# Kernel tuning notes

Measured on AMD Instinct MI355X. Metric: run time of the kernel, lower is better.

The kernel has to match this reference:

```python
import jax, jax.numpy as jnp
import numpy as np

N_NODES = 50000
N_EDGES = 800000
DIM = 128
N_LAYERS = 3
N_GRAPHS = 64
NEG_SLOPE = 0.2


def setup_inputs() -> dict:
    key = jax.random.key(0)
    ks = jax.random.split(key, 9)
    x = jax.random.normal(ks[0], (N_NODES, DIM), dtype=jnp.float32)
    edge_index = jax.random.randint(ks[1], (2, N_EDGES), 0, N_NODES, dtype=jnp.int32)
    batch = jnp.sort(jax.random.randint(ks[2], (N_NODES,), 0, N_GRAPHS, dtype=jnp.int32))
    Ws = jax.random.normal(ks[3], (N_LAYERS, DIM, DIM), dtype=jnp.float32) / np.sqrt(DIM)
    att_src = jax.random.normal(ks[4], (N_LAYERS, DIM), dtype=jnp.float32) * 0.1
    att_dst = jax.random.normal(ks[5], (N_LAYERS, DIM), dtype=jnp.float32) * 0.1
    biases = jnp.zeros((N_LAYERS, DIM), dtype=jnp.float32)
    Wf = jax.random.normal(ks[6], (DIM, 1), dtype=jnp.float32) / np.sqrt(DIM)
    bf = jnp.zeros((1,), dtype=jnp.float32)
    return {"x": x, "edge_index": edge_index, "batch": batch, "Ws": Ws,
            "att_src": att_src, "att_dst": att_dst, "biases": biases,
            "Wf": Wf, "bf": bf}


def _gat_layer(x, src, dst, W, a_src, a_dst, b, n_nodes):
    # PyG GATConv, heads=1: linear transform, per-edge attention, softmax over
    # edges incoming to each dst node, scatter-add aggregation, bias.
    h = x @ W                                        # [N, H]
    alpha = jax.nn.leaky_relu(
        (h * a_src).sum(-1)[src] + (h * a_dst).sum(-1)[dst], NEG_SLOPE)  # [E]
    m = jax.ops.segment_max(alpha, dst, num_segments=n_nodes)
    e = jnp.exp(alpha - m[dst])
    s = jax.ops.segment_sum(e, dst, num_segments=n_nodes)
    w = e / (s[dst] + 1e-16)                         # softmax per dst-neighborhood
    out = jax.ops.segment_sum(w[:, None] * h[src], dst, num_segments=n_nodes)
    return out + b


def reference(x, edge_index, batch, Ws, att_src, att_dst, biases, Wf, bf):
    n_nodes = x.shape[0]
    loop = jnp.arange(n_nodes, dtype=edge_index.dtype)   # add_self_loops=True
    src = jnp.concatenate([edge_index[0], loop])
    dst = jnp.concatenate([edge_index[1], loop])
    for l in range(N_LAYERS):
        x = _gat_layer(x, src, dst, Ws[l], att_src[l], att_dst[l], biases[l], n_nodes)
        x = jax.nn.relu(x)
    pooled = jax.ops.segment_sum(x, batch, num_segments=N_GRAPHS)  # global_add_pool
    y = (pooled @ Wf + bf).squeeze(-1)               # [N_GRAPHS]
    return y
```

## Files before the change

kernel.cpp:

```cpp
#include <hip/hip_runtime.h>
#include <hip/hip_bf16.h>

#define N_NODES 50000
#define DIM 128
#define N_GRAPHS 64
#define E_RAW 800000
#define E_TOT 850000
#define NSLOT 1000000
#define E_CAP 1200000
#define NEG_SLOPE 0.2f
#define PAD_SENT 0xFFFF0000u

typedef unsigned int uint;
typedef unsigned short ushort;
typedef float v2f __attribute__((ext_vector_type(2)));
typedef short bf16x8 __attribute__((ext_vector_type(8)));
typedef float f32x4 __attribute__((ext_vector_type(4)));

__device__ __forceinline__ int pi_pos(int p) {
    return (p >> 3) + 32 * ((p >> 1) & 3) + 16 * (p & 1);
}

__device__ __forceinline__ ushort f2bf(float f) {
    uint u = __float_as_uint(f);
    u += 0x7fffu + ((u >> 16) & 1u);
    return (ushort)(u >> 16);
}

__global__ void init_kernel(int* deg, int* fillc, float* pooled) {
    int i = blockIdx.x * blockDim.x + threadIdx.x;
    if (i < N_NODES) { deg[i] = 0; fillc[i] = 0; }
    if (i < N_GRAPHS * DIM) pooled[i] = 0.f;
}

__global__ void csr_init_kernel(uint* __restrict__ csr) {
    int i = blockIdx.x * blockDim.x + threadIdx.x;
    if (i < NSLOT / 4) ((uint4*)csr)[i] = make_uint4(PAD_SENT, PAD_SENT, PAD_SENT, PAD_SENT);
}

__global__ void x2bf_kernel(const float* __restrict__ x, ushort* __restrict__ xb) {
    int i = blockIdx.x * blockDim.x + threadIdx.x;
    if (i >= N_NODES * DIM / 4) return;
    float4 v = ((const float4*)x)[i];
    ushort4 o;
    o.x = f2bf(v.x); o.y = f2bf(v.y); o.z = f2bf(v.z); o.w = f2bf(v.w);
    ((ushort4*)xb)[i] = o;
}

__global__ void wprep_kernel(const float* __restrict__ Ws, ushort* __restrict__ Wfrag) {
    int t = blockIdx.x * blockDim.x + threadIdx.x;
    if (t >= 3 * 32 * 64) return;
    int l = t >> 11;
    int rem = t & 2047;
    int chunk = rem >> 6, lane = rem & 63;
    int ks = chunk >> 3, nt = chunk & 7;
    int cc = lane & 15, gg = lane >> 4;
    const float* W = Ws + (size_t)l * DIM * DIM;
    ushort o[8];
#pragma unroll
    for (int j = 0; j < 8; ++j) {
        int kp = ks * 32 + gg * 8 + j;
        int kl = (l == 0) ? kp : pi_pos(kp);
        o[j] = f2bf(W[kl * DIM + nt * 16 + cc]);
    }
#pragma unroll
    for (int j = 0; j < 8; ++j) Wfrag[(size_t)t * 8 + j] = o[j];
}

__global__ void count_kernel(const int* __restrict__ ei, int* __restrict__ deg) {
    int e = blockIdx.x * blockDim.x + threadIdx.x;
    if (e >= E_TOT) return;
    int dst = (e < E_RAW) ? ei[E_RAW + e] : (e - E_RAW);
    atomicAdd(&deg[dst], 1);
}

__global__ void scan1_kernel(const int* __restrict__ deg, int* __restrict__ excl,
                             int* __restrict__ blksum, int n) {
    __shared__ int lds[256];
    int t = threadIdx.x;
    int i = blockIdx.x * 256 + t;
    int v = (i < n) ? ((deg[i] + 3) & ~3) : 0;
    lds[t] = v;
    __syncthreads();
    int incl = v;
    for (int off = 1; off < 256; off <<= 1) {
        int y = (t >= off) ? lds[t - off] : 0;
        __syncthreads();
        incl += y;
        lds[t] = incl;
        __syncthreads();
    }
    if (i < n) excl[i] = incl - v;
    if (t == 255) blksum[blockIdx.x] = incl;
}

__global__ void scan2_kernel(int* __restrict__ blksum, int* __restrict__ row_ptr, int nblk) {
    __shared__ int lds[256];
    int t = threadIdx.x;
    int v = (t < nblk) ? blksum[t] : 0;
    lds[t] = v;
    __syncthreads();
    int incl = v;
    for (int off = 1; off < 256; off <<= 1) {
        int y = (t >= off) ? lds[t - off] : 0;
        __syncthreads();
        incl += y;
        lds[t] = incl;
        __syncthreads();
    }
    if (t < nblk) blksum[t] = incl - v;
    if (t == nblk - 1) row_ptr[N_NODES] = incl;
}

__global__ void scan3_kernel(int* __restrict__ row_ptr, const int* __restrict__ blksum, int n) {
    int i = blockIdx.x * blockDim.x + threadIdx.x;
    if (i < n) row_ptr[i] += blksum[i >> 8];
}

__global__ void fill_kernel(const int* __restrict__ ei, const int* __restrict__ row_ptr,
                            int* __restrict__ fillc, uint* __restrict__ csr) {
    int e = blockIdx.x * blockDim.x + threadIdx.x;
    if (e >= E_TOT) return;
    int src, dst;
    if (e < E_RAW) { src = ei[e]; dst = ei[E_RAW + e]; }
    else           { src = dst = e - E_RAW; }
    int slot = row_ptr[dst] + atomicAdd(&fillc[dst], 1);
    csr[slot] = (uint)src | ((uint)dst << 16);
}

__global__ __launch_bounds__(256) void gemm_mfma_kernel(
    const ushort* __restrict__ Xb, const ushort* __restrict__ Wfrag,
    const float* __restrict__ asrc, const float* __restrict__ adst,
    uint* __restrict__ Hb, float* __restrict__ s1, float* __restrict__ s2, int nrows) {
    int wv = threadIdx.x >> 6;
    int lane = threadIdx.x & 63;
    int c = lane & 15, g = lane >> 4;
    int row0 = blockIdx.x * 64 + wv * 16;

    int arow = row0 + c;
    if (arow >= nrows) arow = nrows - 1;
    const ushort* xrow = Xb + (size_t)arow * DIM;

    f32x4 acc[8];
#pragma unroll
    for (int nt = 0; nt < 8; ++nt) acc[nt] = (f32x4)(0.f);

#pragma unroll
    for (int ks = 0; ks < 4; ++ks) {
        bf16x8 afrag = *(const bf16x8*)(xrow + ks * 32 + g * 8);
#pragma unroll
        for (int nt = 0; nt < 8; ++nt) {
            bf16x8 bfrag = *(const bf16x8*)(Wfrag + ((size_t)(ks * 8 + nt) * 64 + lane) * 8);
            acc[nt] = __builtin_amdgcn_mfma_f32_16x16x32_bf16(afrag, bfrag, acc[nt], 0, 0, 0);
        }
    }

    float a1[8], a2[8];
#pragma unroll
    for (int nt = 0; nt < 8; ++nt) { a1[nt] = asrc[c + 16 * nt]; a2[nt] = adst[c + 16 * nt]; }

#pragma unroll
    for (int r = 0; r < 4; ++r) {
        int outrow = row0 + g * 4 + r;
        bool valid = outrow < nrows;
        if (valid) {
            int w0 = __builtin_amdgcn_cvt_pk_fp8_f32(acc[0][r], acc[1][r], 0, false);
            w0     = __builtin_amdgcn_cvt_pk_fp8_f32(acc[2][r], acc[3][r], w0, true);
            int w1 = __builtin_amdgcn_cvt_pk_fp8_f32(acc[4][r], acc[5][r], 0, false);
            w1     = __builtin_amdgcn_cvt_pk_fp8_f32(acc[6][r], acc[7][r], w1, true);
            *(uint2*)&Hb[(size_t)outrow * 32 + c * 2] = make_uint2((uint)w0, (uint)w1);
        }
        float p1 = 0.f, p2 = 0.f;
#pragma unroll
        for (int nt = 0; nt < 8; ++nt) {
            p1 = fmaf(acc[nt][r], a1[nt], p1);
            p2 = fmaf(acc[nt][r], a2[nt], p2);
        }
#pragma unroll
        for (int m = 1; m < 16; m <<= 1) { p1 += __shfl_xor(p1, m); p2 += __shfl_xor(p2, m); }
        if (c == 0 && valid) { s1[outrow] = p1; s2[outrow] = p2; }
    }
}

__global__ __launch_bounds__(256) void ew_kernel(
    const uint* __restrict__ csr, const float* __restrict__ s1,
    const float* __restrict__ s2, float* __restrict__ w) {
    int i = blockIdx.x * blockDim.x + threadIdx.x;
    if (i >= NSLOT / 4) return;
    uint4 e = ((const uint4*)csr)[i];
    uint ev[4] = {e.x, e.y, e.z, e.w};
    float ov[4];
#pragma unroll
    for (int j = 0; j < 4; ++j) {
        uint dv = ev[j] >> 16;
        uint sv = ev[j] & 0xFFFFu;
        float wv = 0.f;
        if (dv != 0xFFFFu) {
            float al = s1[sv] + s2[dv];
            al = fmaxf(al, NEG_SLOPE * al);
            wv = __expf(al);
        }
        ov[j] = wv;
    }
    float4 o;
    o.x = ov[0]; o.y = ov[1]; o.z = ov[2]; o.w = ov[3];
    ((float4*)w)[i] = o;
}

__global__ __launch_bounds__(256) void agg_kernel(
    const uint2* __restrict__ Hb2, const uint* __restrict__ csr,
    const int* __restrict__ row_ptr, const float* __restrict__ w,
    const float* __restrict__ bias,
    ushort* __restrict__ Xout, const int* __restrict__ batch,
    float* __restrict__ pooled, int pool_flag, int ngroups) {
    int gw = (blockIdx.x * blockDim.x + threadIdx.x) >> 6;
    int lane = threadIdx.x & 63;
    if (gw >= ngroups) return;
    int node0 = gw * 8;
    int ql = lane & 15;
    int grp = lane >> 4;

    int4 rpa = *(const int4*)&row_ptr[node0];
    int4 rpb = *(const int4*)&row_ptr[node0 + 4];
    int rp8 = row_ptr[node0 + 8];
    int rp[9] = {rpa.x, rpa.y, rpa.z, rpa.w, rpb.x, rpb.y, rpb.z, rpb.w, rp8};

    int p0 = 8 * ql + 2 * grp;
    float2 b2;
    b2.x = bias[pi_pos(p0)];
    b2.y = bias[pi_pos(p0) + 16];

    int ba[8] = {0, 0, 0, 0, 0, 0, 0, 0};
    if (pool_flag) {
        int4 bqa = *(const int4*)&batch[node0];
        int4 bqb = *(const int4*)&batch[node0 + 4];
        ba[0] = bqa.x; ba[1] = bqa.y; ba[2] = bqa.z; ba[3] = bqa.w;
        ba[4] = bqb.x; ba[5] = bqb.y; ba[6] = bqb.z; ba[7] = bqb.w;
    }

#pragma unroll
    for (int k = 0; k < 8; ++k) {
        int beg = rp[k], end = rp[k + 1];
        float a0 = 0.f, a1 = 0.f, a2 = 0.f, a3 = 0.f;
        float a4 = 0.f, a5 = 0.f, a6 = 0.f, a7 = 0.f, ws = 0.f;

        for (int s = beg; s < end; s += 8) {
            uint4 ca = *(const uint4*)&csr[s];
            float4 wa = *(const float4*)&w[s];
            bool vb = (s + 4) < end;
            uint4 cb = vb ? *(const uint4*)&csr[s + 4]
                          : make_uint4(PAD_SENT, PAD_SENT, PAD_SENT, PAD_SENT);
            float4 wb = vb ? *(const float4*)&w[s + 4] : make_float4(0.f, 0.f, 0.f, 0.f);

            uint  eA = (grp == 0) ? ca.x : (grp == 1) ? ca.y : (grp == 2) ? ca.z : ca.w;
            float wA = (grp == 0) ? wa.x : (grp == 1) ? wa.y : (grp == 2) ? wa.z : wa.w;
            uint  eB = (grp == 0) ? cb.x : (grp == 1) ? cb.y : (grp == 2) ? cb.z : cb.w;
            float wB = (grp == 0) ? wb.x : (grp == 1) ? wb.y : (grp == 2) ? wb.z : wb.w;

            uint2 hA = Hb2[(eA & 0xFFFFu) * 16u + (uint)ql];
            uint2 hB = Hb2[(eB & 0xFFFFu) * 16u + (uint)ql];

            v2f f;
            f = __builtin_amdgcn_cvt_pk_f32_fp8((int)hA.x, false); a0 = fmaf(wA, f.x, a0); a1 = fmaf(wA, f.y, a1);
            f = __builtin_amdgcn_cvt_pk_f32_fp8((int)hA.x, true);  a2 = fmaf(wA, f.x, a2); a3 = fmaf(wA, f.y, a3);
            f = __builtin_amdgcn_cvt_pk_f32_fp8((int)hA.y, false); a4 = fmaf(wA, f.x, a4); a5 = fmaf(wA, f.y, a5);
            f = __builtin_amdgcn_cvt_pk_f32_fp8((int)hA.y, true);  a6 = fmaf(wA, f.x, a6); a7 = fmaf(wA, f.y, a7);
            ws += wA;
            f = __builtin_amdgcn_cvt_pk_f32_fp8((int)hB.x, false); a0 = fmaf(wB, f.x, a0); a1 = fmaf(wB, f.y, a1);
            f = __builtin_amdgcn_cvt_pk_f32_fp8((int)hB.x, true);  a2 = fmaf(wB, f.x, a2); a3 = fmaf(wB, f.y, a3);
            f = __builtin_amdgcn_cvt_pk_f32_fp8((int)hB.y, false); a4 = fmaf(wB, f.x, a4); a5 = fmaf(wB, f.y, a5);
            f = __builtin_amdgcn_cvt_pk_f32_fp8((int)hB.y, true);  a6 = fmaf(wB, f.x, a6); a7 = fmaf(wB, f.y, a7);
            ws += wB;
        }

        a0 += __shfl_xor(a0, 16); a0 += __shfl_xor(a0, 32);
        a1 += __shfl_xor(a1, 16); a1 += __shfl_xor(a1, 32);
        a2 += __shfl_xor(a2, 16); a2 += __shfl_xor(a2, 32);
        a3 += __shfl_xor(a3, 16); a3 += __shfl_xor(a3, 32);
        a4 += __shfl_xor(a4, 16); a4 += __shfl_xor(a4, 32);
        a5 += __shfl_xor(a5, 16); a5 += __shfl_xor(a5, 32);
        a6 += __shfl_xor(a6, 16); a6 += __shfl_xor(a6, 32);
        a7 += __shfl_xor(a7, 16); a7 += __shfl_xor(a7, 32);
        ws += __shfl_xor(ws, 16); ws += __shfl_xor(ws, 32);

        float inv = 1.f / (ws + 1e-16f);
        float vx = (grp == 0) ? a0 : (grp == 1) ? a2 : (grp == 2) ? a4 : a6;
        float vy = (grp == 0) ? a1 : (grp == 1) ? a3 : (grp == 2) ? a5 : a7;
        vx = fmaxf(fmaf(vx, inv, b2.x), 0.f);
        vy = fmaxf(fmaf(vy, inv, b2.y), 0.f);

        if (pool_flag) {
            atomicAdd(&pooled[ba[k] * DIM + p0], vx);
            atomicAdd(&pooled[ba[k] * DIM + p0 + 1], vy);
        } else {
            ushort2 hb;
            hb.x = f2bf(vx);
            hb.y = f2bf(vy);
            ((ushort2*)Xout)[(size_t)(node0 + k) * 64 + (p0 >> 1)] = hb;
        }
    }
}

__global__ void final_kernel(const float* __restrict__ pooled, const float* __restrict__ Wf,
                             const float* __restrict__ bf, float* __restrict__ y) {
    int wid = (blockIdx.x * blockDim.x + threadIdx.x) >> 6;
    int lane = threadIdx.x & 63;
    if (wid >= N_GRAPHS) return;
    float2 p = *(const float2*)&pooled[wid * DIM + 2 * lane];
    int cc = lane >> 2, ii = lane & 3;
    float wx = Wf[cc + 32 * ii];
    float wy = Wf[cc + 32 * ii + 16];
    float v = p.x * wx + p.y * wy;
    for (int off = 32; off; off >>= 1) v += __shfl_down(v, off);
    if (lane == 0) y[wid] = v + bf[0];
}

extern "C" void kernel_launch(void* const* d_in, const int* in_sizes, int n_in,
                              void* d_out, int out_size, void* d_ws, size_t ws_size,
                              hipStream_t stream) {
    const float* x       = (const float*)d_in[0];
    const int*   ei      = (const int*)d_in[1];
    const int*   batch   = (const int*)d_in[2];
    const float* Ws      = (const float*)d_in[3];
    const float* att_src = (const float*)d_in[4];
    const float* att_dst = (const float*)d_in[5];
    const float* biases  = (const float*)d_in[6];
    const float* Wf      = (const float*)d_in[7];
    const float* bf      = (const float*)d_in[8];
    float* y = (float*)d_out;

    char* p = (char*)d_ws;
    auto alloc = [&](size_t bytes) -> void* {
        void* r = (void*)p;
        p += (bytes + 255) & ~(size_t)255;
        return r;
    };
    ushort* xC     = (ushort*)alloc((size_t)(N_NODES + 64) * DIM * 2);
    ushort* xA     = (ushort*)alloc((size_t)(N_NODES + 64) * DIM * 2);
    uint*   Hb     = (uint*)alloc((size_t)N_NODES * 32 * 4);
    ushort* Wfrag  = (ushort*)alloc((size_t)3 * 32 * 64 * 8 * 2);
    uint*  csr     = (uint*)alloc((size_t)E_CAP * 4);
    float* wbuf    = (float*)alloc((size_t)E_CAP * 4);
    int*   deg     = (int*)alloc((size_t)N_NODES * 4);
    int*   fillc   = (int*)alloc((size_t)N_NODES * 4);
    int*   row_ptr = (int*)alloc((size_t)(N_NODES + 16) * 4);
    int*   blksum  = (int*)alloc(256 * 4);
    float* s1      = (float*)alloc((size_t)N_NODES * 4);
    float* s2      = (float*)alloc((size_t)(N_NODES + 8) * 4);
    float* pooled  = (float*)alloc((size_t)N_GRAPHS * DIM * 4);

    const int BN = 256;
    const int gN   = (N_NODES + BN - 1) / BN;
    const int gE   = (E_TOT + BN - 1) / BN;
    const int ngroups = N_NODES / 8;
    const int gAGG = (ngroups * 64 + BN - 1) / BN;
    const int nblk = gN;
    const int gCVT = (N_NODES * DIM / 4 + BN - 1) / BN;
    const int gGEMM = (N_NODES + 63) / 64;
    const int gEW  = (NSLOT / 4 + BN - 1) / BN;
    const int gCI  = (NSLOT / 4 + BN - 1) / BN;

    init_kernel<<<gN, BN, 0, stream>>>(deg, fillc, pooled);
    csr_init_kernel<<<gCI, BN, 0, stream>>>(csr);
    x2bf_kernel<<<gCVT, BN, 0, stream>>>(x, xC);
    wprep_kernel<<<(3 * 32 * 64 + BN - 1) / BN, BN, 0, stream>>>(Ws, Wfrag);
    count_kernel<<<gE, BN, 0, stream>>>(ei, deg);
    scan1_kernel<<<nblk, BN, 0, stream>>>(deg, row_ptr, blksum, N_NODES);
    scan2_kernel<<<1, BN, 0, stream>>>(blksum, row_ptr, nblk);
    scan3_kernel<<<gN, BN, 0, stream>>>(row_ptr, blksum, N_NODES);
    fill_kernel<<<gE, BN, 0, stream>>>(ei, row_ptr, fillc, csr);

    const ushort* xin = xC;
    ushort* xout = xA;
    for (int l = 0; l < 3; ++l) {
        const ushort* Wf_l = Wfrag + (size_t)l * 32 * 64 * 8;
        const float* as = att_src + (size_t)l * DIM;
        const float* ad = att_dst + (size_t)l * DIM;
        const float* b  = biases + (size_t)l * DIM;

        gemm_mfma_kernel<<<gGEMM, BN, 0, stream>>>(xin, Wf_l, as, ad, Hb, s1, s2, N_NODES);
        ew_kernel<<<gEW, BN, 0, stream>>>(csr, s1, s2, wbuf);
        agg_kernel<<<gAGG, BN, 0, stream>>>((const uint2*)Hb, csr, row_ptr, wbuf, b,
                                            xout, batch, pooled,
                                            (l == 2) ? 1 : 0, ngroups);
        xin = xout;
        xout = (l == 0) ? xC : xA;
    }

    final_kernel<<<(N_GRAPHS * 64 + BN - 1) / BN, BN, 0, stream>>>(pooled, Wf, bf, y);
    (void)ws_size; (void)n_in; (void)in_sizes; (void)out_size;
}
```

Before: 354.5 us.

## Pack bf16 edge weight with source index and restructure aggregation loop

The edge-weight kernel now writes a single packed word per edge (source index in the low 16 bits, bf16 weight in the high 16), so the aggregation kernel reads one stream instead of separate csr and weight arrays. The aggregation loop now handles 4 edges per iteration, prefetching the next packed chunk, instead of 8 with a conditional second load. Each wave now covers 4 nodes rather than 8, which doubles the wave count. This cuts edge-stream traffic and the selects for the second chunk, but weights lose precision going to bf16 and there are fewer independent gathers in flight per iteration.

```diff
diff --git a/kernel.cpp b/kernel.cpp
--- a/kernel.cpp
+++ b/kernel.cpp
@@ -184,93 +184,75 @@
 
 __global__ __launch_bounds__(256) void ew_kernel(
     const uint* __restrict__ csr, const float* __restrict__ s1,
-    const float* __restrict__ s2, float* __restrict__ w) {
+    const float* __restrict__ s2, uint* __restrict__ cw) {
     int i = blockIdx.x * blockDim.x + threadIdx.x;
     if (i >= NSLOT / 4) return;
     uint4 e = ((const uint4*)csr)[i];
     uint ev[4] = {e.x, e.y, e.z, e.w};
-    float ov[4];
+    uint ov[4];
 #pragma unroll
     for (int j = 0; j < 4; ++j) {
         uint dv = ev[j] >> 16;
         uint sv = ev[j] & 0xFFFFu;
-        float wv = 0.f;
+        uint out = 0u;
         if (dv != 0xFFFFu) {
             float al = s1[sv] + s2[dv];
             al = fmaxf(al, NEG_SLOPE * al);
-            wv = __expf(al);
-        }
-        ov[j] = wv;
-    }
-    float4 o;
-    o.x = ov[0]; o.y = ov[1]; o.z = ov[2]; o.w = ov[3];
-    ((float4*)w)[i] = o;
+            float wv = __expf(al);
+            out = sv | ((uint)f2bf(wv) << 16);
+        }
+        ov[j] = out;
+    }
+    ((uint4*)cw)[i] = make_uint4(ov[0], ov[1], ov[2], ov[3]);
 }
 
 __global__ __launch_bounds__(256) void agg_kernel(
-    const uint2* __restrict__ Hb2, const uint* __restrict__ csr,
-    const int* __restrict__ row_ptr, const float* __restrict__ w,
-    const float* __restrict__ bias,
+    const uint2* __restrict__ Hb2, const uint* __restrict__ cw,
+    const int* __restrict__ row_ptr, const float* __restrict__ bias,
     ushort* __restrict__ Xout, const int* __restrict__ batch,
     float* __restrict__ pooled, int pool_flag, int ngroups) {
     int gw = (blockIdx.x * blockDim.x + threadIdx.x) >> 6;
     int lane = threadIdx.x & 63;
     if (gw >= ngroups) return;
-    int node0 = gw * 8;
+    int node0 = gw * 4;
     int ql = lane & 15;
     int grp = lane >> 4;
 
     int4 rpa = *(const int4*)&row_ptr[node0];
-    int4 rpb = *(const int4*)&row_ptr[node0 + 4];
-    int rp8 = row_ptr[node0 + 8];
-    int rp[9] = {rpa.x, rpa.y, rpa.z, rpa.w, rpb.x, rpb.y, rpb.z, rpb.w, rp8};
+    int rp4 = row_ptr[node0 + 4];
 
     int p0 = 8 * ql + 2 * grp;
     float2 b2;
     b2.x = bias[pi_pos(p0)];
     b2.y = bias[pi_pos(p0) + 16];
 
-    int ba[8] = {0, 0, 0, 0, 0, 0, 0, 0};
+    int ba0 = 0, ba1 = 0, ba2 = 0, ba3 = 0;
     if (pool_flag) {
-        int4 bqa = *(const int4*)&batch[node0];
-        int4 bqb = *(const int4*)&batch[node0 + 4];
-        ba[0] = bqa.x; ba[1] = bqa.y; ba[2] = bqa.z; ba[3] = bqa.w;
-        ba[4] = bqb.x; ba[5] = bqb.y; ba[6] = bqb.z; ba[7] = bqb.w;
-    }
-
-#pragma unroll
-    for (int k = 0; k < 8; ++k) {
-        int beg = rp[k], end = rp[k + 1];
+        int4 bq = *(const int4*)&batch[node0];
+        ba0 = bq.x; ba1 = bq.y; ba2 = bq.z; ba3 = bq.w;
+    }
+
+    auto seg = [&](int beg, int end, int bk, int node) {
         float a0 = 0.f, a1 = 0.f, a2 = 0.f, a3 = 0.f;
         float a4 = 0.f, a5 = 0.f, a6 = 0.f, a7 = 0.f, ws = 0.f;
 
-        for (int s = beg; s < end; s += 8) {
-            uint4 ca = *(const uint4*)&csr[s];
-            float4 wa = *(const float4*)&w[s];
-            bool vb = (s + 4) < end;
-            uint4 cb = vb ? *(const uint4*)&csr[s + 4]
-                          : make_uint4(PAD_SENT, PAD_SENT, PAD_SENT, PAD_SENT);
-            float4 wb = vb ? *(const float4*)&w[s + 4] : make_float4(0.f, 0.f, 0.f, 0.f);
-
-            uint  eA = (grp == 0) ? ca.x : (grp == 1) ? ca.y : (grp == 2) ? ca.z : ca.w;
-            float wA = (grp == 0) ? wa.x : (grp == 1) ? wa.y : (grp == 2) ? wa.z : wa.w;
-            uint  eB = (grp == 0) ? cb.x : (grp == 1) ? cb.y : (grp == 2) ? cb.z : cb.w;
-            float wB = (grp == 0) ? wb.x : (grp == 1) ? wb.y : (grp == 2) ? wb.z : wb.w;
-
-            uint2 hA = Hb2[(eA & 0xFFFFu) * 16u + (uint)ql];
-            uint2 hB = Hb2[(eB & 0xFFFFu) * 16u + (uint)ql];
+        uint4 cur = *(const uint4*)&cw[beg];
+        for (int s = beg; s < end; s += 4) {
+            int snx = s + 4;
+            snx = (snx < end) ? snx : s;
+            uint4 nxt = *(const uint4*)&cw[snx];
+
+            uint  e  = (grp == 0) ? cur.x : (grp == 1) ? cur.y : (grp == 2) ? cur.z : cur.w;
+            float wv = __uint_as_float(e & 0xFFFF0000u);
+            uint2 hv = Hb2[(e & 0xFFFFu) * 16u + (uint)ql];
 
             v2f f;
-            f = __builtin_amdgcn_cvt_pk_f32_fp8((int)hA.x, false); a0 = fmaf(wA, f.x, a0); a1 = fmaf(wA, f.y, a1);
-            f = __builtin_amdgcn_cvt_pk_f32_fp8((int)hA.x, true);  a2 = fmaf(wA, f.x, a2); a3 = fmaf(wA, f.y, a3);
-            f = __builtin_amdgcn_cvt_pk_f32_fp8((int)hA.y, false); a4 = fmaf(wA, f.x, a4); a5 = fmaf(wA, f.y, a5);
-            f = __builtin_amdgcn_cvt_pk_f32_fp8((int)hA.y, true);  a6 = fmaf(wA, f.x, a6); a7 = fmaf(wA, f.y, a7);
-            ws += wA;
-            f = __builtin_amdgcn_cvt_pk_f32_fp8((int)hB.x, false); a0 = fmaf(wB, f.x, a0); a1 = fmaf(wB, f.y, a1);
-            f = __builtin_amdgcn_cvt_pk_f32_fp8((int)hB.x, true);  a2 = fmaf(wB, f.x, a2); a3 = fmaf(wB, f.y, a3);
-            f = __builtin_amdgcn_cvt_pk_f32_fp8((int)hB.y, false); a4 = fmaf(wB, f.x, a4); a5 = fmaf(wB, f.y, a5);
-            f = __builtin_amdgcn_cvt_pk_f32_fp8((int)hB.y, true);  a6 = fmaf(wB, f.x, a6); a7 = fmaf(wB, f.y, a7);
-            ws += wB;
+            f = __builtin_amdgcn_cvt_pk_f32_fp8((int)hv.x, false); a0 = fmaf(wv, f.x, a0); a1 = fmaf(wv, f.y, a1);
+            f = __builtin_amdgcn_cvt_pk_f32_fp8((int)hv.x, true);  a2 = fmaf(wv, f.x, a2); a3 = fmaf(wv, f.y, a3);
+            f = __builtin_amdgcn_cvt_pk_f32_fp8((int)hv.y, false); a4 = fmaf(wv, f.x, a4); a5 = fmaf(wv, f.y, a5);
+            f = __builtin_amdgcn_cvt_pk_f32_fp8((int)hv.y, true);  a6 = fmaf(wv, f.x, a6); a7 = fmaf(wv, f.y, a7);
+            ws += wv;
+            cur = nxt;
         }
 
         a0 += __shfl_xor(a0, 16); a0 += __shfl_xor(a0, 32);
@@ -290,15 +272,20 @@
         vy = fmaxf(fmaf(vy, inv, b2.y), 0.f);
 
         if (pool_flag) {
-            atomicAdd(&pooled[ba[k] * DIM + p0], vx);
-            atomicAdd(&pooled[ba[k] * DIM + p0 + 1], vy);
+            atomicAdd(&pooled[bk * DIM + p0], vx);
+            atomicAdd(&pooled[bk * DIM + p0 + 1], vy);
         } else {
             ushort2 hb;
             hb.x = f2bf(vx);
             hb.y = f2bf(vy);
-            ((ushort2*)Xout)[(size_t)(node0 + k) * 64 + (p0 >> 1)] = hb;
-        }
-    }
+            ((ushort2*)Xout)[(size_t)node * 64 + (p0 >> 1)] = hb;
+        }
+    };
+
+    seg(rpa.x, rpa.y, ba0, node0);
+    seg(rpa.y, rpa.z, ba1, node0 + 1);
+    seg(rpa.z, rpa.w, ba2, node0 + 2);
+    seg(rpa.w, rp4,  ba3, node0 + 3);
 }
 
 __global__ void final_kernel(const float* __restrict__ pooled, const float* __restrict__ Wf,
@@ -340,7 +327,7 @@
     uint*   Hb     = (uint*)alloc((size_t)N_NODES * 32 * 4);
     ushort* Wfrag  = (ushort*)alloc((size_t)3 * 32 * 64 * 8 * 2);
     uint*  csr     = (uint*)alloc((size_t)E_CAP * 4);
-    float* wbuf    = (float*)alloc((size_t)E_CAP * 4);
+    uint*  cwbuf   = (uint*)alloc((size_t)E_CAP * 4);
     int*   deg     = (int*)alloc((size_t)N_NODES * 4);
     int*   fillc   = (int*)alloc((size_t)N_NODES * 4);
     int*   row_ptr = (int*)alloc((size_t)(N_NODES + 16) * 4);
@@ -352,7 +339,7 @@
     const int BN = 256;
     const int gN   = (N_NODES + BN - 1) / BN;
     const int gE   = (E_TOT + BN - 1) / BN;
-    const int ngroups = N_NODES / 8;
+    const int ngroups = N_NODES / 4;
     const int gAGG = (ngroups * 64 + BN - 1) / BN;
     const int nblk = gN;
     const int gCVT = (N_NODES * DIM / 4 + BN - 1) / BN;
@@ -379,8 +366,8 @@
         const float* b  = biases + (size_t)l * DIM;
 
         gemm_mfma_kernel<<<gGEMM, BN, 0, stream>>>(xin, Wf_l, as, ad, Hb, s1, s2, N_NODES);
-        ew_kernel<<<gEW, BN, 0, stream>>>(csr, s1, s2, wbuf);
-        agg_kernel<<<gAGG, BN, 0, stream>>>((const uint2*)Hb, csr, row_ptr, wbuf, b,
+        ew_kernel<<<gEW, BN, 0, stream>>>(csr, s1, s2, cwbuf);
+        agg_kernel<<<gAGG, BN, 0, stream>>>((const uint2*)Hb, cwbuf, row_ptr, b,
                                             xout, batch, pooled,
                                             (l == 2) ? 1 : 0, ngroups);
         xin = xout;
```

Result: slower. 387.2 us (+9.2%).
